# Kernel tuning notes

Measured on AMD Instinct MI355X. Metric: run time of the kernel, lower is better.

The kernel has to match this reference:

```python
import jax, jax.numpy as jnp
import numpy as np

DILATIONS = [1, 2, 4, 8, 16, 32, 64, 128]
DEC_LEN = 256  # decoder_seq_len


def conv1x1(x, w, b):
    # x: [B, C, T], w: [O, C], b: [O]
    return jnp.einsum('oc,bct->bot', w, x) + b[None, :, None]


def causal_conv(x, w, b, dil):
    # x: [B, C, T], w: [O, C, K]; left-pad by (K-1)*dil => causal, same T out
    pad = (w.shape[-1] - 1) * dil
    y = jax.lax.conv_general_dilated(
        x, w, window_strides=(1,), padding=[(pad, 0)], rhs_dilation=(dil,),
        dimension_numbers=('NCH', 'OIH', 'NCH'))
    return y + b[None, :, None]


def setup_inputs() -> dict:
    key = jax.random.key(0)
    ks = jax.random.split(key, 14)
    L, Cin, Cout, Cmid, K, P = 8, 32, 64, 64, 2, 128
    B, T = 32, 4096
    s = 0.05  # keep activations in a sane range
    return {
        'x': jax.random.normal(ks[0], (B, Cin, T), dtype=jnp.float32),
        'pre_w': jax.random.normal(ks[1], (L, Cout, Cin)) * s,
        'pre_b': jax.random.normal(ks[2], (L, Cout)) * s,
        'filt_w': jax.random.normal(ks[3], (L, Cmid, Cout, K)) * s,
        'filt_b': jax.random.normal(ks[4], (L, Cmid)) * s,
        'gate_w': jax.random.normal(ks[5], (L, Cmid, Cout, K)) * s,
        'gate_b': jax.random.normal(ks[6], (L, Cmid)) * s,
        'post_w': jax.random.normal(ks[7], (L, Cout, Cmid)) * s,
        'post_b': jax.random.normal(ks[8], (L, Cout)) * s,
        'd1_w': jax.random.normal(ks[9], (P, Cout)) * s,
        'd1_b': jax.random.normal(ks[10], (P,)) * s,
        'd2_w': jax.random.normal(ks[11], (1, P)) * s,
        'd2_b': jax.random.normal(ks[12], (1,)) * s,
        'teacher_forcing_ratio': 1,
    }


def reference(x, pre_w, pre_b, filt_w, filt_b, gate_w, gate_b,
              post_w, post_b, d1_w, d1_b, d2_w, d2_b, teacher_forcing_ratio):
    # teacher_forcing_ratio == 1 path (vectorized teacher-forced forward)
    acc = None
    for i, dil in enumerate(DILATIONS):  # fixed small set of branches
        h = jax.nn.relu(conv1x1(x, pre_w[i], pre_b[i]))          # DenseConv pre
        f = causal_conv(h, filt_w[i], filt_b[i], dil)             # filter
        g = causal_conv(h, gate_w[i], gate_b[i], dil)             # gate
        s = jnp.tanh(f) * jax.nn.relu(g)                          # gated activation
        p = jax.nn.relu(conv1x1(s, post_w[i], post_b[i]))         # DenseConv post (skip output)
        acc = p if acc is None else acc + p
    out = jax.nn.relu(conv1x1(acc, d1_w, d1_b))                   # conv_dense1 (dropout=eval no-op)
    out = jax.nn.relu(conv1x1(out, d2_w, d2_b))                   # conv_dense2 -> [B, 1, T]
    out = jnp.transpose(out, (0, 2, 1))                           # [B, T, 1]
    return out[:, -DEC_LEN:, :]
```

## Files before the change

kernel.cpp:

```cpp
#include <hip/hip_runtime.h>

typedef _Float16 half2_t __attribute__((ext_vector_type(2)));
typedef _Float16 f16x8 __attribute__((ext_vector_type(8)));
typedef float f32x4 __attribute__((ext_vector_type(4)));

#define DEC 256
#define TFULL 4096
#define WIN0 3584
#define WLAYER_U32 11264
#define WTOT_U32 (8 * WLAYER_U32)
#define X16_U32 (32 * 512 * 16)
#define P_U32 (8 * 256 * 1024)
#define XP_U32 (WTOT_U32 + X16_U32)
#define WS_NEED2 ((size_t)(XP_U32 + P_U32) * 4)

#define HSTR 36
#define SSTR 36
#define HU (64 * HSTR)
#define LDS_U32 (HU + 32 * SSTR)

__device__ __forceinline__ float fast_tanh(float x) {
    float xa = fminf(fmaxf(x, -10.f), 10.f);
    float e = __expf(2.f * xa);
    return (e - 1.f) * __builtin_amdgcn_rcpf(e + 1.f);
}
__device__ __forceinline__ unsigned pk_rte(float a, float b) {
    union { _Float16 h[2]; unsigned u; } v;
    v.h[0] = (_Float16)a; v.h[1] = (_Float16)b; return v.u;
}
__device__ __forceinline__ half2_t h2(unsigned u) {
    return __builtin_bit_cast(half2_t, u);
}
__device__ __forceinline__ unsigned pkrtz(float a, float b) {
    return __builtin_bit_cast(unsigned, __builtin_amdgcn_cvt_pkrtz(a, b));
}

__global__ __launch_bounds__(512) void wavenet_prep16(
    const float* __restrict__ x,
    const float* __restrict__ pre_w,
    const float* __restrict__ fw, const float* __restrict__ gw,
    const float* __restrict__ pw, unsigned* __restrict__ ws)
{
    int idx = blockIdx.x * 512 + threadIdx.x;
    if (idx >= XP_U32) return;
    unsigned v;
    if (idx < WTOT_U32) {
        int i = idx / WLAYER_U32;
        int r = idx - i * WLAYER_U32;
        if (r < 1024) {
            int kg = r >> 8, o = (r >> 2) & 63, e = r & 3;
            const float* p = pre_w + (i * 64 + o) * 32 + 8 * kg + 2 * e;
            v = pk_rte(p[0], p[1]);
        } else if (r < 9216) {
            const int isg = (r >= 5120);
            int e2 = r - (isg ? 5120 : 1024);
            int kb = e2 >> 8, o = (e2 >> 2) & 63, e = e2 & 3;
            int m = kb >> 2, h4g = kb & 3;
            int tap = m >> 1;
            int c = 32 * (m & 1) + 8 * h4g + 2 * e;
            const float* src = isg ? gw : fw;
            const float* p = src + ((i * 64 + o) * 64 + c) * 2 + tap;
            v = pk_rte(p[0], p[2]);
        } else {
            int e3 = r - 9216;
            int kg = e3 >> 8, o = (e3 >> 2) & 63, e = e3 & 3;
            const float* p = pw + (i * 64 + o) * 64 + 8 * kg + 2 * e;
            v = pk_rte(p[0], p[1]);
        }
    } else {
        int e = idx - WTOT_U32;
        int b = e >> 13, r2 = e & 8191;
        int tw = r2 >> 4, cp = r2 & 15;
        const float* p = x + (size_t)(b * 32 + 2 * cp) * TFULL + WIN0 + tw;
        v = pk_rte(p[0], p[TFULL]);
    }
    ws[idx] = v;
}

__global__ __launch_bounds__(512) void wavenet_mfma2(
    const unsigned* __restrict__ wsu,
    const float* __restrict__ pre_b,
    const float* __restrict__ filt_b, const float* __restrict__ gate_b,
    const float* __restrict__ post_b,
    unsigned* __restrict__ pout)
{
    __shared__ __align__(16) unsigned lds[LDS_U32];

    const int tid = threadIdx.x;
    const int i = blockIdx.x >> 8;
    const int bt = blockIdx.x & 255;
    const int b = bt >> 3;
    const int tile = bt & 7;
    const int dil = 1 << i;
    const int off1 = (dil < 32) ? dil : 32;
    const int t0 = TFULL - DEC + tile * 32;

    const int lane = tid & 63;
    const int wv = __builtin_amdgcn_readfirstlane(tid >> 6);
    const int h4 = lane >> 4;
    const int ln = lane & 15;
    const int mt = wv >> 1;
    const int nt = wv & 1;

    const unsigned* xw = wsu + WTOT_U32 + b * 8192;
    const unsigned* wl = wsu + i * WLAYER_U32;

    {
        f16x8 a = *(const f16x8*)(wl + (h4 * 64 + mt * 16 + ln) * 4);
        float4 pb4 = *(const float4*)(pre_b + i * 64 + mt * 16 + 4 * h4);
#pragma unroll
        for (int ct2 = 0; ct2 < 2; ++ct2) {
            const int cw = (2 * nt + ct2) * 16 + ln;
            int ta = (dil >= 32) ? ((cw < 32) ? (t0 - dil + cw) : (t0 + cw - 32))
                                 : (t0 - dil + cw);
            const int tw = (ta - WIN0) & 511;
            f16x8 bx = *(const f16x8*)(xw + tw * 16 + h4 * 4);
            f32x4 c = {0.f, 0.f, 0.f, 0.f};
            c = __builtin_amdgcn_mfma_f32_16x16x32_f16(a, bx, c, 0, 0, 0);
            uint2 hv;
            hv.x = pkrtz(fmaxf(c[0] + pb4.x, 0.f), fmaxf(c[1] + pb4.y, 0.f));
            hv.y = pkrtz(fmaxf(c[2] + pb4.z, 0.f), fmaxf(c[3] + pb4.w, 0.f));
            *(uint2*)&lds[cw * HSTR + mt * 8 + h4 * 2] = hv;
        }
    }
    __syncthreads();

    const int t = nt * 16 + ln;

    {
        f32x4 cf = {0.f, 0.f, 0.f, 0.f};
        f32x4 cg = {0.f, 0.f, 0.f, 0.f};
        const unsigned* fA = wl + 1024;
        const unsigned* gA = wl + 5120;
#pragma unroll
        for (int m = 0; m < 4; ++m) {
            const int kbg = 4 * m + h4;
            const int row = (m >> 1) ? (t + off1) : t;
            uint4 bf = *(const uint4*)&lds[row * HSTR + 16 * (m & 1) + 4 * h4];
            f16x8 bfrag = __builtin_bit_cast(f16x8, bf);
            f16x8 af = *(const f16x8*)(fA + (kbg * 64 + mt * 16 + ln) * 4);
            f16x8 ag = *(const f16x8*)(gA + (kbg * 64 + mt * 16 + ln) * 4);
            cf = __builtin_amdgcn_mfma_f32_16x16x32_f16(af, bfrag, cf, 0, 0, 0);
            cg = __builtin_amdgcn_mfma_f32_16x16x32_f16(ag, bfrag, cg, 0, 0, 0);
        }
        float4 fb = *(const float4*)(filt_b + i * 64 + mt * 16 + 4 * h4);
        float4 gb = *(const float4*)(gate_b + i * 64 + mt * 16 + 4 * h4);
        float s0 = fast_tanh(cf[0] + fb.x) * fmaxf(cg[0] + gb.x, 0.f);
        float s1 = fast_tanh(cf[1] + fb.y) * fmaxf(cg[1] + gb.y, 0.f);
        float s2 = fast_tanh(cf[2] + fb.z) * fmaxf(cg[2] + gb.z, 0.f);
        float s3 = fast_tanh(cf[3] + fb.w) * fmaxf(cg[3] + gb.w, 0.f);
        uint2 sv;
        sv.x = pkrtz(s0, s1);
        sv.y = pkrtz(s2, s3);
        *(uint2*)&lds[HU + t * SSTR + mt * 8 + h4 * 2] = sv;
    }
    __syncthreads();

    {
        f32x4 cp = {0.f, 0.f, 0.f, 0.f};
        const unsigned* pA = wl + 9216;
#pragma unroll
        for (int ki = 0; ki < 2; ++ki) {
            const int kg = 4 * ki + h4;
            f16x8 bs = *(const f16x8*)&lds[HU + t * SSTR + 4 * kg];
            f16x8 ap = *(const f16x8*)(pA + (kg * 64 + mt * 16 + ln) * 4);
            cp = __builtin_amdgcn_mfma_f32_16x16x32_f16(ap, bs, cp, 0, 0, 0);
        }
        float4 pb = *(const float4*)(post_b + i * 64 + mt * 16 + 4 * h4);
        uint2 o2;
        o2.x = pkrtz(fmaxf(cp[0] + pb.x, 0.f), fmaxf(cp[1] + pb.y, 0.f));
        o2.y = pkrtz(fmaxf(cp[2] + pb.z, 0.f), fmaxf(cp[3] + pb.w, 0.f));
        unsigned* po = pout + (size_t)(i * 256 + bt) * 1024;
        *(uint2*)&po[(mt * 4 + h4) * 64 + 2 * t] = o2;
    }
}

__global__ __launch_bounds__(512) void wavenet_head16(
    const unsigned* __restrict__ pin,
    const float* __restrict__ d1_w, const float* __restrict__ d1_b,
    const float* __restrict__ d2_w, const float* __restrict__ d2_b,
    float* __restrict__ out)
{
    __shared__ __align__(16) float accf[64 * 33];
    __shared__ float red[512];
    const int tid = threadIdx.x;
    const int bt = blockIdx.x;
    const int q = tid >> 5, tt = tid & 31;

    float a[4] = {0.f, 0.f, 0.f, 0.f};
#pragma unroll
    for (int l = 0; l < 8; ++l) {
        const unsigned* p = pin + (size_t)(l * 256 + bt) * 1024;
        uint2 u = *(const uint2*)&p[q * 64 + 2 * tt];
        half2_t u0 = h2(u.x), u1 = h2(u.y);
        a[0] += (float)u0[0]; a[1] += (float)u0[1];
        a[2] += (float)u1[0]; a[3] += (float)u1[1];
    }
#pragma unroll
    for (int oo = 0; oo < 4; ++oo) accf[(4 * q + oo) * 33 + tt] = a[oo];
    __syncthreads();

    {
        const int pg = tid >> 5;
        float partial = 0.f;
#pragma unroll
        for (int pp = 0; pp < 8; ++pp) {
            const int p = pg * 8 + pp;
            float z = d1_b[p];
            const float4* w4 = (const float4*)(d1_w + p * 64);
#pragma unroll 4
            for (int c4 = 0; c4 < 16; ++c4) {
                float4 w = w4[c4];
                z = fmaf(w.x, accf[(c4 * 4 + 0) * 33 + tt], z);
                z = fmaf(w.y, accf[(c4 * 4 + 1) * 33 + tt], z);
                z = fmaf(w.z, accf[(c4 * 4 + 2) * 33 + tt], z);
                z = fmaf(w.w, accf[(c4 * 4 + 3) * 33 + tt], z);
            }
            partial = fmaf(d2_w[p], fmaxf(z, 0.f), partial);
        }
        red[pg * 32 + tt] = partial;
    }
    __syncthreads();
    if (tid < 32) {
        float sum = d2_b[0];
#pragma unroll
        for (int g = 0; g < 16; ++g) sum += red[g * 32 + tid];
        out[bt * 32 + tid] = fmaxf(sum, 0.f);
    }
}

#define HROW 164
#define SROW 33
__global__ __launch_bounds__(512) void wavenet_main(
    const float* __restrict__ x,
    const float* __restrict__ pre_w, const float* __restrict__ pre_b,
    const float* __restrict__ filt_w, const float* __restrict__ filt_b,
    const float* __restrict__ gate_w, const float* __restrict__ gate_b,
    const float* __restrict__ post_w, const float* __restrict__ post_b,
    const float* __restrict__ d1_w, const float* __restrict__ d1_b,
    const float* __restrict__ d2_w, const float* __restrict__ d2_b,
    float* __restrict__ out)
{
    __shared__ __align__(16) float h_s[64 * HROW];
    __shared__ __align__(16) float wbuf[20480];
    __shared__ __align__(16) float s_s[64 * SROW];
    const int tid = threadIdx.x;
    const int b = blockIdx.x >> 3;
    const int tile = blockIdx.x & 7;
    const int t0 = TFULL - DEC + tile * 32;
    const int lane = tid & 63;
    const int wv = __builtin_amdgcn_readfirstlane(tid >> 6);
    const int q = tid >> 5;
    const int tt = tid & 31;
    float accp[4] = {0.f, 0.f, 0.f, 0.f};
    for (int i = 0; i < 8; ++i) {
        const int dil = 1 << i;
        const int NC = 32 + dil;
        for (int m = tid; m < 8192; m += 512) {
            int c = m >> 7, rem = m & 127, o = rem >> 1, k = m & 1;
            wbuf[m] = filt_w[((i * 64 + o) * 64 + c) * 2 + k];
            wbuf[8192 + m] = gate_w[((i * 64 + o) * 64 + c) * 2 + k];
        }
        for (int m = tid; m < 4096; m += 512) {
            int c = m >> 6, o = m & 63;
            wbuf[16384 + m] = post_w[(i * 64 + o) * 64 + c];
        }
        __syncthreads();
        {
            const float* preb = pre_b + i * 64 + wv * 8;
            const float* prew = pre_w + (i * 64 + wv * 8) * 32;
            for (int col = lane; col < NC; col += 64) {
                int ta = t0 - dil + col;
                const float* xp = x + (size_t)b * 32 * TFULL + ta;
                float hacc[8];
#pragma unroll
                for (int r = 0; r < 8; ++r) hacc[r] = preb[r];
                for (int ci = 0; ci < 32; ++ci) {
                    float xv = xp[ci * TFULL];
#pragma unroll
                    for (int r = 0; r < 8; ++r)
                        hacc[r] = fmaf(prew[r * 32 + ci], xv, hacc[r]);
                }
#pragma unroll
                for (int r = 0; r < 8; ++r)
                    h_s[(wv * 8 + r) * HROW + col] = fmaxf(hacc[r], 0.f);
            }
        }
        __syncthreads();
        {
            float fa[4], ga[4];
#pragma unroll
            for (int oo = 0; oo < 4; ++oo) {
                fa[oo] = filt_b[i * 64 + q * 4 + oo];
                ga[oo] = gate_b[i * 64 + q * 4 + oo];
            }
            const float4* fw4 = (const float4*)wbuf;
            const float4* gw4 = (const float4*)(wbuf + 8192);
            const float* hrow0 = h_s + tt;
            const float* hrow1 = h_s + tt + dil;
#pragma unroll 4
            for (int c = 0; c < 64; ++c) {
                float4 f0 = fw4[c * 32 + q * 2];
                float4 f1 = fw4[c * 32 + q * 2 + 1];
                float4 g0 = gw4[c * 32 + q * 2];
                float4 g1 = gw4[c * 32 + q * 2 + 1];
                float h0 = hrow0[c * HROW];
                float h1 = hrow1[c * HROW];
                fa[0] = fmaf(f0.x, h0, fmaf(f0.y, h1, fa[0]));
                fa[1] = fmaf(f0.z, h0, fmaf(f0.w, h1, fa[1]));
                fa[2] = fmaf(f1.x, h0, fmaf(f1.y, h1, fa[2]));
                fa[3] = fmaf(f1.z, h0, fmaf(f1.w, h1, fa[3]));
                ga[0] = fmaf(g0.x, h0, fmaf(g0.y, h1, ga[0]));
                ga[1] = fmaf(g0.z, h0, fmaf(g0.w, h1, ga[1]));
                ga[2] = fmaf(g1.x, h0, fmaf(g1.y, h1, ga[2]));
                ga[3] = fmaf(g1.z, h0, fmaf(g1.w, h1, ga[3]));
            }
#pragma unroll
            for (int oo = 0; oo < 4; ++oo)
                s_s[(q * 4 + oo) * SROW + tt] = fast_tanh(fa[oo]) * fmaxf(ga[oo], 0.f);
        }
        __syncthreads();
        {
            float pa[4];
#pragma unroll
            for (int oo = 0; oo < 4; ++oo) pa[oo] = post_b[i * 64 + q * 4 + oo];
            const float4* pw4 = (const float4*)(wbuf + 16384);
#pragma unroll 4
            for (int c = 0; c < 64; ++c) {
                float4 pv = pw4[c * 16 + q];
                float sv = s_s[c * SROW + tt];
                pa[0] = fmaf(pv.x, sv, pa[0]);
                pa[1] = fmaf(pv.y, sv, pa[1]);
                pa[2] = fmaf(pv.z, sv, pa[2]);
                pa[3] = fmaf(pv.w, sv, pa[3]);
            }
#pragma unroll
            for (int oo = 0; oo < 4; ++oo) accp[oo] += fmaxf(pa[oo], 0.f);
        }
        __syncthreads();
    }
#pragma unroll
    for (int oo = 0; oo < 4; ++oo) s_s[(q * 4 + oo) * SROW + tt] = accp[oo];
    __syncthreads();
    {
        const int pg = tid >> 5;
        float partial = 0.f;
#pragma unroll
        for (int pp = 0; pp < 8; ++pp) {
            const int p = pg * 8 + pp;
            float z = d1_b[p];
            const float4* w4 = (const float4*)(d1_w + p * 64);
#pragma unroll 4
            for (int c4 = 0; c4 < 16; ++c4) {
                float4 w = w4[c4];
                z = fmaf(w.x, s_s[(c4 * 4 + 0) * SROW + tt], z);
                z = fmaf(w.y, s_s[(c4 * 4 + 1) * SROW + tt], z);
                z = fmaf(w.z, s_s[(c4 * 4 + 2) * SROW + tt], z);
                z = fmaf(w.w, s_s[(c4 * 4 + 3) * SROW + tt], z);
            }
            partial = fmaf(d2_w[p], fmaxf(z, 0.f), partial);
        }
        h_s[pg * 32 + tt] = partial;
    }
    __syncthreads();
    if (tid < 32) {
        float sum = d2_b[0];
#pragma unroll
        for (int g = 0; g < 16; ++g) sum += h_s[g * 32 + tid];
        out[b * DEC + tile * 32 + tid] = fmaxf(sum, 0.f);
    }
}

extern "C" void kernel_launch(void* const* d_in, const int* in_sizes, int n_in,
                              void* d_out, int out_size, void* d_ws, size_t ws_size,
                              hipStream_t stream)
{
    const float* x      = (const float*)d_in[0];
    const float* pre_w  = (const float*)d_in[1];
    const float* pre_b  = (const float*)d_in[2];
    const float* filt_w = (const float*)d_in[3];
    const float* filt_b = (const float*)d_in[4];
    const float* gate_w = (const float*)d_in[5];
    const float* gate_b = (const float*)d_in[6];
    const float* post_w = (const float*)d_in[7];
    const float* post_b = (const float*)d_in[8];
    const float* d1_w   = (const float*)d_in[9];
    const float* d1_b   = (const float*)d_in[10];
    const float* d2_w   = (const float*)d_in[11];
    const float* d2_b   = (const float*)d_in[12];
    float* out = (float*)d_out;

    if (ws_size >= WS_NEED2) {
        unsigned* ws = (unsigned*)d_ws;
        unsigned* part = ws + XP_U32;
        wavenet_prep16<<<688, 512, 0, stream>>>(x, pre_w, filt_w, gate_w, post_w, ws);
        wavenet_mfma2<<<2048, 512, 0, stream>>>(
            ws, pre_b, filt_b, gate_b, post_b, part);
        wavenet_head16<<<256, 512, 0, stream>>>(
            part, d1_w, d1_b, d2_w, d2_b, out);
    } else {
        wavenet_main<<<256, 512, 0, stream>>>(
            x, pre_w, pre_b, filt_w, filt_b, gate_w, gate_b, post_w, post_b,
            d1_w, d1_b, d2_w, d2_b, out);
    }
}
```

Baseline: 30.65 us.

## Fuse layer loop and dense head into one kernel with 8-step time tiles

Replaces the per-layer MFMA kernel and separate head kernel with a single kernel where each block handles one batch and 8 output timesteps. It loops over all 8 dilated layers, accumulates the skip sum in registers, and runs the dense head in-block. This removes one launch and the global round-trip of per-layer fp16 partial outputs. The cost is more __syncthreads per block, half-empty MFMA tiles (only 8 of 16 columns used), redundant loads of per-layer weights, and fewer total blocks (1024 versus 2048).

After: 39.53 us. +29.0%, slower.

```diff
diff --git a/kernel.cpp b/kernel.cpp
--- a/kernel.cpp
+++ b/kernel.cpp
@@ -10,14 +10,11 @@
 #define WLAYER_U32 11264
 #define WTOT_U32 (8 * WLAYER_U32)
 #define X16_U32 (32 * 512 * 16)
-#define P_U32 (8 * 256 * 1024)
 #define XP_U32 (WTOT_U32 + X16_U32)
-#define WS_NEED2 ((size_t)(XP_U32 + P_U32) * 4)
-
-#define HSTR 36
-#define SSTR 36
-#define HU (64 * HSTR)
-#define LDS_U32 (HU + 32 * SSTR)
+#define WS_NEED ((size_t)XP_U32 * 4)
+
+#define EXCH_U32 1536
+#define LDS1_U32 2560
 
 __device__ __forceinline__ float fast_tanh(float x) {
     float xa = fminf(fmaxf(x, -10.f), 10.f);
@@ -77,155 +74,160 @@
     ws[idx] = v;
 }
 
-__global__ __launch_bounds__(512) void wavenet_mfma2(
+__global__ __launch_bounds__(512) void wavenet_one(
     const unsigned* __restrict__ wsu,
     const float* __restrict__ pre_b,
     const float* __restrict__ filt_b, const float* __restrict__ gate_b,
     const float* __restrict__ post_b,
-    unsigned* __restrict__ pout)
+    const float* __restrict__ d1_w, const float* __restrict__ d1_b,
+    const float* __restrict__ d2_w, const float* __restrict__ d2_b,
+    float* __restrict__ out)
 {
-    __shared__ __align__(16) unsigned lds[LDS_U32];
+    __shared__ __align__(16) unsigned lds[LDS1_U32];
+    float* exch = (float*)(lds + EXCH_U32);
 
     const int tid = threadIdx.x;
-    const int i = blockIdx.x >> 8;
-    const int bt = blockIdx.x & 255;
-    const int b = bt >> 3;
-    const int tile = bt & 7;
-    const int dil = 1 << i;
-    const int off1 = (dil < 32) ? dil : 32;
-    const int t0 = TFULL - DEC + tile * 32;
+    const int b = blockIdx.x >> 5;
+    const int tq = blockIdx.x & 31;
+    const int t0 = TFULL - DEC + tq * 8;
 
     const int lane = tid & 63;
     const int wv = __builtin_amdgcn_readfirstlane(tid >> 6);
     const int h4 = lane >> 4;
     const int ln = lane & 15;
+    const int tt = ln & 7;
+
+    const unsigned* xw = wsu + WTOT_U32 + b * 8192;
+
     const int mt = wv >> 1;
-    const int nt = wv & 1;
-
-    const unsigned* xw = wsu + WTOT_U32 + b * 8192;
-    const unsigned* wl = wsu + i * WLAYER_U32;
-
-    {
-        f16x8 a = *(const f16x8*)(wl + (h4 * 64 + mt * 16 + ln) * 4);
-        float4 pb4 = *(const float4*)(pre_b + i * 64 + mt * 16 + 4 * h4);
-#pragma unroll
-        for (int ct2 = 0; ct2 < 2; ++ct2) {
-            const int cw = (2 * nt + ct2) * 16 + ln;
-            int ta = (dil >= 32) ? ((cw < 32) ? (t0 - dil + cw) : (t0 + cw - 32))
-                                 : (t0 - dil + cw);
-            const int tw = (ta - WIN0) & 511;
+    const int fg = wv & 1;
+
+    float acc[4] = {0.f, 0.f, 0.f, 0.f};
+
+    for (int i = 0; i < 8; ++i) {
+        const int dil = 1 << i;
+        const unsigned* wl = wsu + i * WLAYER_U32;
+
+        if (wv < 4) {
+            const int m1 = wv;
+            f16x8 a = *(const f16x8*)(wl + (h4 * 64 + m1 * 16 + ln) * 4);
+            float4 pb4 = *(const float4*)(pre_b + i * 64 + m1 * 16 + 4 * h4);
+            const int ta = (ln < 8) ? (t0 - dil + ln) : (t0 + ln - 8);
+            const int tw = ta - WIN0;
             f16x8 bx = *(const f16x8*)(xw + tw * 16 + h4 * 4);
             f32x4 c = {0.f, 0.f, 0.f, 0.f};
             c = __builtin_amdgcn_mfma_f32_16x16x32_f16(a, bx, c, 0, 0, 0);
             uint2 hv;
             hv.x = pkrtz(fmaxf(c[0] + pb4.x, 0.f), fmaxf(c[1] + pb4.y, 0.f));
             hv.y = pkrtz(fmaxf(c[2] + pb4.z, 0.f), fmaxf(c[3] + pb4.w, 0.f));
-            *(uint2*)&lds[cw * HSTR + mt * 8 + h4 * 2] = hv;
-        }
+            *(uint2*)&lds[ln * 36 + m1 * 8 + h4 * 2] = hv;
+        }
+        __syncthreads();
+
+        f32x4 cv = {0.f, 0.f, 0.f, 0.f};
+        {
+            const unsigned* wA = wl + (fg ? 5120 : 1024);
+#pragma unroll
+            for (int m = 0; m < 4; ++m) {
+                const int kbg = 4 * m + h4;
+                const int row = (m >> 1) ? (8 + tt) : tt;
+                uint4 bf4 = *(const uint4*)&lds[row * 36 + 16 * (m & 1) + 4 * h4];
+                f16x8 bfrag = __builtin_bit_cast(f16x8, bf4);
+                f16x8 af = *(const f16x8*)(wA + (kbg * 64 + mt * 16 + ln) * 4);
+                cv = __builtin_amdgcn_mfma_f32_16x16x32_f16(af, bfrag, cv, 0, 0, 0);
+            }
+        }
+        if (fg && ln < 8) {
+#pragma unroll
+            for (int r = 0; r < 4; ++r)
+                exch[(mt * 16 + 4 * h4 + r) * 9 + tt] = cv[r];
+        }
+        __syncthreads();
+        if (!fg && ln < 8) {
+            float4 fb = *(const float4*)(filt_b + i * 64 + mt * 16 + 4 * h4);
+            float4 gb = *(const float4*)(gate_b + i * 64 + mt * 16 + 4 * h4);
+            const int o0 = mt * 16 + 4 * h4;
+            float g0 = exch[(o0 + 0) * 9 + tt] + gb.x;
+            float g1 = exch[(o0 + 1) * 9 + tt] + gb.y;
+            float g2 = exch[(o0 + 2) * 9 + tt] + gb.z;
+            float g3 = exch[(o0 + 3) * 9 + tt] + gb.w;
+            float s0 = fast_tanh(cv[0] + fb.x) * fmaxf(g0, 0.f);
+            float s1 = fast_tanh(cv[1] + fb.y) * fmaxf(g1, 0.f);
+            float s2 = fast_tanh(cv[2] + fb.z) * fmaxf(g2, 0.f);
+            float s3 = fast_tanh(cv[3] + fb.w) * fmaxf(g3, 0.f);
+            uint2 sv;
+            sv.x = pkrtz(s0, s1);
+            sv.y = pkrtz(s2, s3);
+            *(uint2*)&lds[576 + tt * 36 + mt * 8 + h4 * 2] = sv;
+        }
+        __syncthreads();
+
+        {
+            const int kg = 4 * fg + h4;
+            uint4 bs4 = *(const uint4*)&lds[576 + tt * 36 + 4 * kg];
+            f16x8 bs = __builtin_bit_cast(f16x8, bs4);
+            f16x8 ap = *(const f16x8*)(wl + 9216 + (kg * 64 + mt * 16 + ln) * 4);
+            f32x4 cp = {0.f, 0.f, 0.f, 0.f};
+            cp = __builtin_amdgcn_mfma_f32_16x16x32_f16(ap, bs, cp, 0, 0, 0);
+            if (!fg && ln < 8) {
+#pragma unroll
+                for (int r = 0; r < 4; ++r)
+                    exch[(mt * 16 + 4 * h4 + r) * 9 + tt] = cp[r];
+            }
+            __syncthreads();
+            if (fg) {
+                float4 pb = *(const float4*)(post_b + i * 64 + mt * 16 + 4 * h4);
+                const int o0 = mt * 16 + 4 * h4;
+                acc[0] += fmaxf(cp[0] + exch[(o0 + 0) * 9 + tt] + pb.x, 0.f);
+                acc[1] += fmaxf(cp[1] + exch[(o0 + 1) * 9 + tt] + pb.y, 0.f);
+                acc[2] += fmaxf(cp[2] + exch[(o0 + 2) * 9 + tt] + pb.z, 0.f);
+                acc[3] += fmaxf(cp[3] + exch[(o0 + 3) * 9 + tt] + pb.w, 0.f);
+            }
+        }
+    }
+
+    if (fg && ln < 8) {
+#pragma unroll
+        for (int r = 0; r < 4; ++r)
+            exch[(mt * 16 + 4 * h4 + r) * 9 + tt] = acc[r];
     }
     __syncthreads();
 
-    const int t = nt * 16 + ln;
-
+    float* zbuf = (float*)lds;
+    float* red = (float*)(lds + 1024);
     {
-        f32x4 cf = {0.f, 0.f, 0.f, 0.f};
-        f32x4 cg = {0.f, 0.f, 0.f, 0.f};
-        const unsigned* fA = wl + 1024;
-        const unsigned* gA = wl + 5120;
-#pragma unroll
-        for (int m = 0; m < 4; ++m) {
-            const int kbg = 4 * m + h4;
-            const int row = (m >> 1) ? (t + off1) : t;
-            uint4 bf = *(const uint4*)&lds[row * HSTR + 16 * (m & 1) + 4 * h4];
-            f16x8 bfrag = __builtin_bit_cast(f16x8, bf);
-            f16x8 af = *(const f16x8*)(fA + (kbg * 64 + mt * 16 + ln) * 4);
-            f16x8 ag = *(const f16x8*)(gA + (kbg * 64 + mt * 16 + ln) * 4);
-            cf = __builtin_amdgcn_mfma_f32_16x16x32_f16(af, bfrag, cf, 0, 0, 0);
-            cg = __builtin_amdgcn_mfma_f32_16x16x32_f16(ag, bfrag, cg, 0, 0, 0);
-        }
-        float4 fb = *(const float4*)(filt_b + i * 64 + mt * 16 + 4 * h4);
-        float4 gb = *(const float4*)(gate_b + i * 64 + mt * 16 + 4 * h4);
-        float s0 = fast_tanh(cf[0] + fb.x) * fmaxf(cg[0] + gb.x, 0.f);
-        float s1 = fast_tanh(cf[1] + fb.y) * fmaxf(cg[1] + gb.y, 0.f);
-        float s2 = fast_tanh(cf[2] + fb.z) * fmaxf(cg[2] + gb.z, 0.f);
-        float s3 = fast_tanh(cf[3] + fb.w) * fmaxf(cg[3] + gb.w, 0.f);
-        uint2 sv;
-        sv.x = pkrtz(s0, s1);
-        sv.y = pkrtz(s2, s3);
-        *(uint2*)&lds[HU + t * SSTR + mt * 8 + h4 * 2] = sv;
-    }
-    __syncthreads();
-
-    {
-        f32x4 cp = {0.f, 0.f, 0.f, 0.f};
-        const unsigned* pA = wl + 9216;
-#pragma unroll
-        for (int ki = 0; ki < 2; ++ki) {
-            const int kg = 4 * ki + h4;
-            f16x8 bs = *(const f16x8*)&lds[HU + t * SSTR + 4 * kg];
-            f16x8 ap = *(const f16x8*)(pA + (kg * 64 + mt * 16 + ln) * 4);
-            cp = __builtin_amdgcn_mfma_f32_16x16x32_f16(ap, bs, cp, 0, 0, 0);
-        }
-        float4 pb = *(const float4*)(post_b + i * 64 + mt * 16 + 4 * h4);
-        uint2 o2;
-        o2.x = pkrtz(fmaxf(cp[0] + pb.x, 0.f), fmaxf(cp[1] + pb.y, 0.f));
-        o2.y = pkrtz(fmaxf(cp[2] + pb.z, 0.f), fmaxf(cp[3] + pb.w, 0.f));
-        unsigned* po = pout + (size_t)(i * 256 + bt) * 1024;
-        *(uint2*)&po[(mt * 4 + h4) * 64 + 2 * t] = o2;
-    }
-}
-
-__global__ __launch_bounds__(512) void wavenet_head16(
-    const unsigned* __restrict__ pin,
-    const float* __restrict__ d1_w, const float* __restrict__ d1_b,
-    const float* __restrict__ d2_w, const float* __restrict__ d2_b,
-    float* __restrict__ out)
-{
-    __shared__ __align__(16) float accf[64 * 33];
-    __shared__ float red[512];
-    const int tid = threadIdx.x;
-    const int bt = blockIdx.x;
-    const int q = tid >> 5, tt = tid & 31;
-
-    float a[4] = {0.f, 0.f, 0.f, 0.f};
-#pragma unroll
-    for (int l = 0; l < 8; ++l) {
-        const unsigned* p = pin + (size_t)(l * 256 + bt) * 1024;
-        uint2 u = *(const uint2*)&p[q * 64 + 2 * tt];
-        half2_t u0 = h2(u.x), u1 = h2(u.y);
-        a[0] += (float)u0[0]; a[1] += (float)u0[1];
-        a[2] += (float)u1[0]; a[3] += (float)u1[1];
-    }
-#pragma unroll
-    for (int oo = 0; oo < 4; ++oo) accf[(4 * q + oo) * 33 + tt] = a[oo];
-    __syncthreads();
-
-    {
-        const int pg = tid >> 5;
-        float partial = 0.f;
-#pragma unroll
-        for (int pp = 0; pp < 8; ++pp) {
-            const int p = pg * 8 + pp;
+#pragma unroll
+        for (int k = 0; k < 2; ++k) {
+            const int j = tid + 512 * k;
+            const int p = j >> 3, tc = j & 7;
             float z = d1_b[p];
             const float4* w4 = (const float4*)(d1_w + p * 64);
 #pragma unroll 4
             for (int c4 = 0; c4 < 16; ++c4) {
                 float4 w = w4[c4];
-                z = fmaf(w.x, accf[(c4 * 4 + 0) * 33 + tt], z);
-                z = fmaf(w.y, accf[(c4 * 4 + 1) * 33 + tt], z);
-                z = fmaf(w.z, accf[(c4 * 4 + 2) * 33 + tt], z);
-                z = fmaf(w.w, accf[(c4 * 4 + 3) * 33 + tt], z);
-            }
-            partial = fmaf(d2_w[p], fmaxf(z, 0.f), partial);
-        }
-        red[pg * 32 + tt] = partial;
+                z = fmaf(w.x, exch[(c4 * 4 + 0) * 9 + tc], z);
+                z = fmaf(w.y, exch[(c4 * 4 + 1) * 9 + tc], z);
+                z = fmaf(w.z, exch[(c4 * 4 + 2) * 9 + tc], z);
+                z = fmaf(w.w, exch[(c4 * 4 + 3) * 9 + tc], z);
+            }
+            zbuf[p * 8 + tc] = fmaxf(z, 0.f) * d2_w[p];
+        }
     }
     __syncthreads();
-    if (tid < 32) {
+    if (tid < 64) {
+        const int tc = tid & 7, seg = tid >> 3;
+        float sum = 0.f;
+#pragma unroll
+        for (int k = 0; k < 16; ++k)
+            sum += zbuf[(seg * 16 + k) * 8 + tc];
+        red[tc * 8 + seg] = sum;
+    }
+    __syncthreads();
+    if (tid < 8) {
         float sum = d2_b[0];
 #pragma unroll
-        for (int g = 0; g < 16; ++g) sum += red[g * 32 + tid];
-        out[bt * 32 + tid] = fmaxf(sum, 0.f);
+        for (int g = 0; g < 8; ++g) sum += red[tid * 8 + g];
+        out[b * DEC + tq * 8 + tid] = fmaxf(sum, 0.f);
     }
 }
 
@@ -390,14 +392,11 @@
     const float* d2_b   = (const float*)d_in[12];
     float* out = (float*)d_out;
 
-    if (ws_size >= WS_NEED2) {
+    if (ws_size >= WS_NEED) {
         unsigned* ws = (unsigned*)d_ws;
-        unsigned* part = ws + XP_U32;
         wavenet_prep16<<<688, 512, 0, stream>>>(x, pre_w, filt_w, gate_w, post_w, ws);
-        wavenet_mfma2<<<2048, 512, 0, stream>>>(
-            ws, pre_b, filt_b, gate_b, post_b, part);
-        wavenet_head16<<<256, 512, 0, stream>>>(
-            part, d1_w, d1_b, d2_w, d2_b, out);
+        wavenet_one<<<1024, 512, 0, stream>>>(
+            ws, pre_b, filt_b, gate_b, post_b, d1_w, d1_b, d2_w, d2_b, out);
     } else {
         wavenet_main<<<256, 512, 0, stream>>>(
             x, pre_w, pre_b, filt_w, filt_b, gate_w, gate_b, post_w, post_b,
```
